# Kernel optimization log

Hardware: AMD Instinct MI355X
Metric: run time of the kernel (lower is better)

Reference implementation:

```python
import jax, jax.numpy as jnp
import numpy as np

B, S, MV = 32, 64, 30
V, E, H, L = 20000, 256, 512, 128
PAD_IDX = 0
THETA = 0.5


def setup_inputs() -> dict:
    key = jax.random.key(0)
    ks = jax.random.split(key, 12)
    sc = 0.02
    return {
        "z": jax.random.normal(ks[0], (B, L), jnp.float32),
        "input_sequence": jax.random.randint(ks[1], (B, S, MV), 0, V),
        "length": jax.random.randint(ks[2], (B,), 1, S + 1),
        "embedding_weight": jax.random.normal(ks[3], (V, E), jnp.float32) * sc,
        "W_l2h": jax.random.normal(ks[4], (H, L), jnp.float32) * sc,
        "b_l2h": jax.random.normal(ks[5], (H,), jnp.float32) * sc,
        "W_ih": jax.random.normal(ks[6], (3 * H, E), jnp.float32) * sc,
        "W_hh": jax.random.normal(ks[7], (3 * H, H), jnp.float32) * sc,
        "b_ih": jax.random.normal(ks[8], (3 * H,), jnp.float32) * sc,
        "b_hh": jax.random.normal(ks[9], (3 * H,), jnp.float32) * sc,
        "W_out": jax.random.normal(ks[10], (V, H), jnp.float32) * sc,
        "b_out": jax.random.normal(ks[11], (V,), jnp.float32) * sc,
    }


def _gru(emb, h0, W_ih, W_hh, b_ih, b_hh):
    # emb: (B,S,E); PyTorch GRU cell, single layer.
    def step(h, x_t):
        gi = x_t @ W_ih.T + b_ih          # (B,3H)
        gh = h @ W_hh.T + b_hh            # (B,3H)
        i_r, i_z, i_n = jnp.split(gi, 3, axis=-1)
        h_r, h_z, h_n = jnp.split(gh, 3, axis=-1)
        r = jax.nn.sigmoid(i_r + h_r)
        zt = jax.nn.sigmoid(i_z + h_z)
        n = jnp.tanh(i_n + r * h_n)
        h_new = (1.0 - zt) * n + zt * h
        return h_new, h_new
    _, outs = jax.lax.scan(step, h0, jnp.swapaxes(emb, 0, 1))  # (S,B,H)
    return jnp.swapaxes(outs, 0, 1)  # (B,S,H)


def reference(z, input_sequence, length, embedding_weight, W_l2h, b_l2h,
              W_ih, W_hh, b_ih, b_hh, W_out, b_out):
    # Multi-hot scatter: zeros.scatter_(2, idx, 1)
    mh = jnp.zeros((B, S, V), jnp.float32).at[
        jnp.arange(B)[:, None, None], jnp.arange(S)[None, :, None], input_sequence
    ].set(1.0)
    mh = mh.at[:, :, PAD_IDX].set(0.0)
    # Dense one-hot matmul embedding-sum (faithful to torch.mm on (B*S,V))
    emb = jnp.tanh(jnp.einsum('bsv,ve->bse', mh, embedding_weight))
    h0 = z @ W_l2h.T + b_l2h                      # (B,H)
    outputs = _gru(emb, h0, W_ih, W_hh, b_ih, b_hh)  # (B,S,H)
    # pack/pad semantics: outputs beyond each length are zero
    valid = jnp.arange(S)[None, :] < length[:, None]
    outputs = outputs * valid[..., None]
    m_output = jnp.sum(jnp.abs(outputs), axis=2) > 0  # (B,S) bool
    logits = jnp.einsum('bsh,vh->bsv', outputs, W_out) + b_out  # (B,S,V)
    p_output = jax.nn.sigmoid(logits)
    # _sample: top-k over logits[..., 3:], shift by 3, threshold via sigmoid
    top_p, top_i = jax.lax.top_k(logits[..., 3:], MV)
    top_i = top_i + 3
    s_output = jnp.where(jax.nn.sigmoid(top_p) <= THETA, PAD_IDX, top_i)  # (B,S,MV)
    return (p_output, s_output, m_output)
```

## Files before the change

### kernel.cpp

```cpp
#include <hip/hip_runtime.h>
#include <hip/hip_bf16.h>
#include <math.h>

#define B_ 32
#define S_ 64
#define MV_ 30
#define V_ 20000
#define E_ 256
#define H_ 512
#define L_ 128
#define H3_ 1536
#define BS_ 2048
#define NB4 256
#define NEG7 -3.0e38f
#define SENT 0xFFF8000000000000ULL

typedef __attribute__((ext_vector_type(8))) short short8v;
typedef __attribute__((ext_vector_type(4))) float f32x4;
typedef unsigned long long ull_;

__global__ __launch_bounds__(256) void k12(const int* __restrict__ seq,
                                           const float* __restrict__ Ew,
                                           const float* __restrict__ z,
                                           const float* __restrict__ Wl,
                                           const float* __restrict__ bl,
                                           double* __restrict__ emb,
                                           double* __restrict__ hstep) {
    __shared__ int sidx[MV_];
    int bid = blockIdx.x;
    int t = threadIdx.x;
    if (bid < BS_) {
        int row = bid;
        if (t < MV_) sidx[t] = seq[row * MV_ + t];
        __syncthreads();
        double acc = 0.0;
        for (int i = 0; i < MV_; ++i) {
            int id = sidx[i];
            if (id == 0) continue;
            bool dup = false;
            for (int q = 0; q < i; ++q) dup = dup || (sidx[q] == id);
            if (!dup) acc += (double)Ew[(size_t)id * E_ + t];
        }
        emb[(size_t)row * E_ + t] = tanh(acc);
    } else if (bid < BS_ + 64) {
        int o = (bid - BS_) * 256 + t;
        int b = o >> 9;
        int j = o & 511;
        const float4* zr = (const float4*)(z + (size_t)b * L_);
        const float4* wr = (const float4*)(Wl + (size_t)j * L_);
        double acc = (double)bl[j];
#pragma unroll
        for (int k = 0; k < L_ / 4; ++k) {
            float4 a = zr[k];
            float4 w = wr[k];
            acc += (double)a.x * (double)w.x + (double)a.y * (double)w.y
                 + (double)a.z * (double)w.z + (double)a.w * (double)w.w;
        }
        hstep[(size_t)(b >> 2) * 2048 + j * 4 + (b & 3)] = acc;
    } else {
        ull_* hs = (ull_*)hstep;
        size_t i = (size_t)(bid - (BS_ + 64)) * 1024 + (size_t)t * 4;
        hs[16384 + i + 0] = SENT;
        hs[16384 + i + 1] = SENT;
        hs[16384 + i + 2] = SENT;
        hs[16384 + i + 3] = SENT;
    }
}

__global__ __launch_bounds__(256) void k3_gi(const double* __restrict__ A,
                                             const float* __restrict__ Bm,
                                             const float* __restrict__ bih,
                                             double* __restrict__ gi) {
    __shared__ double As[16][66];
    __shared__ double Bs[16][66];
    int t = threadIdx.x;
    int n0 = blockIdx.x * 64;
    int m0 = blockIdx.y * 64;
    int tx = t & 15, ty = t >> 4;
    int ml = t >> 2;
    int kl = (t & 3) * 4;
    double acc[4][4];
#pragma unroll
    for (int i = 0; i < 4; ++i)
#pragma unroll
        for (int j = 0; j < 4; ++j) acc[i][j] = 0.0;

    for (int kt = 0; kt < 256; kt += 16) {
        double4 av = *(const double4*)(A + (size_t)(m0 + ml) * 256 + kt + kl);
        float4 bv = *(const float4*)(Bm + (size_t)(n0 + ml) * 256 + kt + kl);
        As[kl + 0][ml] = av.x; As[kl + 1][ml] = av.y; As[kl + 2][ml] = av.z; As[kl + 3][ml] = av.w;
        Bs[kl + 0][ml] = (double)bv.x; Bs[kl + 1][ml] = (double)bv.y;
        Bs[kl + 2][ml] = (double)bv.z; Bs[kl + 3][ml] = (double)bv.w;
        __syncthreads();
#pragma unroll
        for (int kk = 0; kk < 16; ++kk) {
            double2 a01 = *(const double2*)&As[kk][ty * 4];
            double2 a23 = *(const double2*)&As[kk][ty * 4 + 2];
            double2 b01 = *(const double2*)&Bs[kk][tx * 4];
            double2 b23 = *(const double2*)&Bs[kk][tx * 4 + 2];
            double am[4] = {a01.x, a01.y, a23.x, a23.y};
            double bn[4] = {b01.x, b01.y, b23.x, b23.y};
#pragma unroll
            for (int i = 0; i < 4; ++i)
#pragma unroll
                for (int j = 0; j < 4; ++j) acc[i][j] += am[i] * bn[j];
        }
        __syncthreads();
    }
#pragma unroll
    for (int i = 0; i < 4; ++i) {
        int m = m0 + ty * 4 + i;
        int bb = m >> 6, ss = m & 63;
#pragma unroll
        for (int j = 0; j < 4; ++j) {
            int n = n0 + tx * 4 + j;
            int g = n >> 9, u = n & 511;
            gi[(((size_t)(ss * 512 + u)) * 3 + g) * 32 + bb] = acc[i][j] + (double)bih[n];
        }
    }
}

__global__ __launch_bounds__(256, 1) void k4_gru(const double* __restrict__ gi,
                                                 const float* __restrict__ whh,
                                                 const float* __restrict__ bhh,
                                                 const int* __restrict__ length,
                                                 double* __restrict__ hstep,
                                                 float* __restrict__ outs) {
    __shared__ double hl[2112];
    __shared__ double part[2][4][16][13];

    int t = threadIdx.x;
    int wv = t >> 6;
    int lane = t & 63;
    int bid = blockIdx.x;
    int g = bid & 7;
    int beta = bid >> 3;

    int ul = lane >> 2, ks = lane & 3;

    const float* wbase = whh + ((size_t)(beta * 16 + ul)) * 512 + wv * 128 + ks * 32;
    float4 w0r[8], w1r[8], w2r[8];
#pragma unroll
    for (int c = 0; c < 8; ++c) {
        w0r[c] = *(const float4*)(wbase + c * 4);
        w1r[c] = *(const float4*)(wbase + 512 * 512 + c * 4);
        w2r[c] = *(const float4*)(wbase + 1024 * 512 + c * 4);
    }

    const double* hg0 = hstep + (size_t)g * 2048;
    {
#pragma unroll
        for (int j = 0; j < 8; ++j) {
            int e = t + j * 256;
            hl[e + ((e >> 7) << 2)] = hg0[e];
        }
    }
    __syncthreads();

    int u2 = lane >> 2, b2 = lane & 3;
    int u_g = beta * 16 + u2;
    int b_g = g * 4 + b2;
    double gr = 0.0, gz = 0.0, gn = 0.0, bhr_ = 0.0, bhz_ = 0.0, bhn_ = 0.0;
    double hv = 0.0;
    int len = 0;
    if (wv == 0) {
        bhr_ = (double)bhh[u_g];
        bhz_ = (double)bhh[u_g + 512];
        bhn_ = (double)bhh[u_g + 1024];
        len = length[b_g];
        hv = hg0[u_g * 4 + b2];
        size_t gb = ((size_t)u_g * 3) * 32 + b_g;
        gr = gi[gb]; gz = gi[gb + 32]; gn = gi[gb + 64];
    }

    const double* hr = &hl[(wv * 128 + ks * 32) * 4 + ((wv * 4 + ks) << 2)];

    for (int s = 0; s < S_; ++s) {
        int par = s & 1;
        double a0[4] = {0, 0, 0, 0}, a1[4] = {0, 0, 0, 0}, a2[4] = {0, 0, 0, 0};
#pragma unroll
        for (int c = 0; c < 8; ++c) {
            const double* hp = hr + c * 16;
            double2 hA0 = *(const double2*)(hp + 0),  hB0 = *(const double2*)(hp + 2);
            double2 hA1 = *(const double2*)(hp + 4),  hB1 = *(const double2*)(hp + 6);
            double2 hA2 = *(const double2*)(hp + 8),  hB2 = *(const double2*)(hp + 10);
            double2 hA3 = *(const double2*)(hp + 12), hB3 = *(const double2*)(hp + 14);
            float4 w0 = w0r[c], w1 = w1r[c], w2 = w2r[c];
            { double d0 = (double)w0.x, d1 = (double)w1.x, d2 = (double)w2.x;
              a0[0] += hA0.x * d0; a0[1] += hA0.y * d0; a0[2] += hB0.x * d0; a0[3] += hB0.y * d0;
              a1[0] += hA0.x * d1; a1[1] += hA0.y * d1; a1[2] += hB0.x * d1; a1[3] += hB0.y * d1;
              a2[0] += hA0.x * d2; a2[1] += hA0.y * d2; a2[2] += hB0.x * d2; a2[3] += hB0.y * d2; }
            { double d0 = (double)w0.y, d1 = (double)w1.y, d2 = (double)w2.y;
              a0[0] += hA1.x * d0; a0[1] += hA1.y * d0; a0[2] += hB1.x * d0; a0[3] += hB1.y * d0;
              a1[0] += hA1.x * d1; a1[1] += hA1.y * d1; a1[2] += hB1.x * d1; a1[3] += hB1.y * d1;
              a2[0] += hA1.x * d2; a2[1] += hA1.y * d2; a2[2] += hB1.x * d2; a2[3] += hB1.y * d2; }
            { double d0 = (double)w0.z, d1 = (double)w1.z, d2 = (double)w2.z;
              a0[0] += hA2.x * d0; a0[1] += hA2.y * d0; a0[2] += hB2.x * d0; a0[3] += hB2.y * d0;
              a1[0] += hA2.x * d1; a1[1] += hA2.y * d1; a1[2] += hB2.x * d1; a1[3] += hB2.y * d1;
              a2[0] += hA2.x * d2; a2[1] += hA2.y * d2; a2[2] += hB2.x * d2; a2[3] += hB2.y * d2; }
            { double d0 = (double)w0.w, d1 = (double)w1.w, d2 = (double)w2.w;
              a0[0] += hA3.x * d0; a0[1] += hA3.y * d0; a0[2] += hB3.x * d0; a0[3] += hB3.y * d0;
              a1[0] += hA3.x * d1; a1[1] += hA3.y * d1; a1[2] += hB3.x * d1; a1[3] += hB3.y * d1;
              a2[0] += hA3.x * d2; a2[1] += hA3.y * d2; a2[2] += hB3.x * d2; a2[3] += hB3.y * d2; }
        }
#pragma unroll
        for (int b = 0; b < 4; ++b) {
            a0[b] += __shfl_xor(a0[b], 1); a0[b] += __shfl_xor(a0[b], 2);
            a1[b] += __shfl_xor(a1[b], 1); a1[b] += __shfl_xor(a1[b], 2);
            a2[b] += __shfl_xor(a2[b], 1); a2[b] += __shfl_xor(a2[b], 2);
        }
        if (ks == 0) {
#pragma unroll
            for (int b = 0; b < 4; ++b) {
                part[par][wv][ul][0 * 4 + b] = a0[b];
                part[par][wv][ul][1 * 4 + b] = a1[b];
                part[par][wv][ul][2 * 4 + b] = a2[b];
            }
        }
        __syncthreads();

        if (wv == 0) {
            double s0 = part[par][0][u2][0 * 4 + b2] + part[par][1][u2][0 * 4 + b2]
                      + part[par][2][u2][0 * 4 + b2] + part[par][3][u2][0 * 4 + b2];
            double s1 = part[par][0][u2][1 * 4 + b2] + part[par][1][u2][1 * 4 + b2]
                      + part[par][2][u2][1 * 4 + b2] + part[par][3][u2][1 * 4 + b2];
            double s2 = part[par][0][u2][2 * 4 + b2] + part[par][1][u2][2 * 4 + b2]
                      + part[par][2][u2][2 * 4 + b2] + part[par][3][u2][2 * 4 + b2];
            double r  = 1.0 / (1.0 + exp(-(gr + s0 + bhr_)));
            double zt = 1.0 / (1.0 + exp(-(gz + s1 + bhz_)));
            double n  = tanh(gn + r * (s2 + bhn_));
            double hn_ = (1.0 - zt) * n + zt * hv;
            hv = hn_;
            if (s < S_ - 1) {
                ull_* hdst = (ull_*)(hstep + (size_t)(s + 1) * 16384 + (size_t)g * 2048);
                __hip_atomic_store(&hdst[beta * 64 + lane],
                                   __builtin_bit_cast(ull_, hn_),
                                   __ATOMIC_RELAXED, __HIP_MEMORY_SCOPE_AGENT);
                size_t gb = ((size_t)((s + 1) * 512 + u_g) * 3) * 32 + b_g;
                gr = gi[gb]; gz = gi[gb + 32]; gn = gi[gb + 64];
            }
            outs[(size_t)(b_g * 64 + s) * H_ + u_g] = (s < len) ? (float)hn_ : 0.0f;
        }
        if (s == S_ - 1) break;

        {
            const ull_* src = (const ull_*)(hstep + (size_t)(s + 1) * 16384
                                            + (size_t)g * 2048) + wv * 512;
            ull_ tmp[8];
            while (true) {
                bool ok = true;
#pragma unroll
                for (int j = 0; j < 8; ++j) {
                    tmp[j] = __hip_atomic_load(&src[j * 64 + lane],
                                               __ATOMIC_RELAXED, __HIP_MEMORY_SCOPE_AGENT);
                    ok = ok && (tmp[j] != SENT);
                }
                if (__all(ok)) break;
                __builtin_amdgcn_s_sleep(1);
            }
            asm volatile("" ::: "memory");
            ull_* hlu = (ull_*)hl;
#pragma unroll
            for (int j = 0; j < 8; ++j) {
                int e = wv * 512 + j * 64 + lane;
                hlu[e + ((e >> 7) << 2)] = tmp[j];
            }
        }
    }
}

__device__ __forceinline__ unsigned short f2b_(float x) {
    unsigned u = __builtin_bit_cast(unsigned, x);
    return (unsigned short)((u + 0x7FFFu + ((u >> 16) & 1u)) >> 16);
}
__device__ __forceinline__ short8v pack8_(float4 a, float4 b) {
    short8v r;
    r[0] = (short)f2b_(a.x); r[1] = (short)f2b_(a.y);
    r[2] = (short)f2b_(a.z); r[3] = (short)f2b_(a.w);
    r[4] = (short)f2b_(b.x); r[5] = (short)f2b_(b.y);
    r[6] = (short)f2b_(b.z); r[7] = (short)f2b_(b.w);
    return r;
}
__global__ __launch_bounds__(256) void k_prep2(const float* __restrict__ Wsrc,
                                               const float* __restrict__ Asrc,
                                               short* __restrict__ W16,
                                               short* __restrict__ A16) {
    int bid = blockIdx.x, t = threadIdx.x;
    if (bid < 5000) {
        int i = bid * 256 + t;
        float4 a = *(const float4*)&Wsrc[(size_t)i * 8];
        float4 b = *(const float4*)&Wsrc[(size_t)i * 8 + 4];
        *(short8v*)&W16[(size_t)i * 8] = pack8_(a, b);
    } else {
        int i = (bid - 5000) * 256 + t;
        float4 a = *(const float4*)&Asrc[(size_t)i * 8];
        float4 b = *(const float4*)&Asrc[(size_t)i * 8 + 4];
        *(short8v*)&A16[(size_t)i * 8] = pack8_(a, b);
    }
}

#define LDK5 72
__global__ __launch_bounds__(256, 2) void k5_mfma(const short* __restrict__ A16,
                                                  const short* __restrict__ W16,
                                                  const float* __restrict__ bo,
                                                  float* __restrict__ pOut) {
    __shared__ short As[128 * LDK5];
    __shared__ short Bs[128 * LDK5];
    int t = threadIdx.x;
    int bid = blockIdx.x;
    int swz = (bid & 7) * 314 + (bid >> 3);
    int m0 = (swz & 15) * 128;
    int n0 = (swz >> 4) * 128;
    int lane = t & 63, wv = t >> 6;
    int wr = wv >> 1, wc = wv & 1;
    int ml = t >> 1;
    int kl = (t & 1) * 32;

    const short* Arow = A16 + (size_t)(m0 + ml) * H_ + kl;
    int vrow = n0 + ml;
    bool vok = vrow < V_;
    const short* Wrow = W16 + (size_t)(vok ? vrow : 0) * H_ + kl;
    short8v zz = (short8v){0, 0, 0, 0, 0, 0, 0, 0};

    f32x4 acc[4][4];
#pragma unroll
    for (int i = 0; i < 4; ++i)
#pragma unroll
        for (int j = 0; j < 4; ++j) acc[i][j] = (f32x4){0.f, 0.f, 0.f, 0.f};

    int ko = lane >> 4;
    int rr = lane & 15;

    for (int kt = 0; kt < H_; kt += 64) {
        short8v a0 = *(const short8v*)(Arow + kt);
        short8v a1 = *(const short8v*)(Arow + kt + 8);
        short8v a2 = *(const short8v*)(Arow + kt + 16);
        short8v a3 = *(const short8v*)(Arow + kt + 24);
        short8v b0 = vok ? *(const short8v*)(Wrow + kt) : zz;
        short8v b1 = vok ? *(const short8v*)(Wrow + kt + 8) : zz;
        short8v b2 = vok ? *(const short8v*)(Wrow + kt + 16) : zz;
        short8v b3 = vok ? *(const short8v*)(Wrow + kt + 24) : zz;
        *(short8v*)&As[ml * LDK5 + kl]      = a0;
        *(short8v*)&As[ml * LDK5 + kl + 8]  = a1;
        *(short8v*)&As[ml * LDK5 + kl + 16] = a2;
        *(short8v*)&As[ml * LDK5 + kl + 24] = a3;
        *(short8v*)&Bs[ml * LDK5 + kl]      = b0;
        *(short8v*)&Bs[ml * LDK5 + kl + 8]  = b1;
        *(short8v*)&Bs[ml * LDK5 + kl + 16] = b2;
        *(short8v*)&Bs[ml * LDK5 + kl + 24] = b3;
        __syncthreads();

#pragma unroll
        for (int kh = 0; kh < 2; ++kh) {
            short8v af[4], bf[4];
#pragma unroll
            for (int i = 0; i < 4; ++i)
                af[i] = *(const short8v*)&As[(wr * 64 + i * 16 + rr) * LDK5 + kh * 32 + ko * 8];
#pragma unroll
            for (int j = 0; j < 4; ++j)
                bf[j] = *(const short8v*)&Bs[(wc * 64 + j * 16 + rr) * LDK5 + kh * 32 + ko * 8];
#pragma unroll
            for (int i = 0; i < 4; ++i)
#pragma unroll
                for (int j = 0; j < 4; ++j)
                    acc[i][j] = __builtin_amdgcn_mfma_f32_16x16x32_bf16(af[i], bf[j], acc[i][j], 0, 0, 0);
        }
        __syncthreads();
    }

    int cr4 = (lane >> 4) * 4;
    float bov[4];
#pragma unroll
    for (int j = 0; j < 4; ++j) {
        int v = n0 + wc * 64 + j * 16 + rr;
        bov[j] = (v < V_) ? bo[v] : 0.f;
    }
#pragma unroll
    for (int i = 0; i < 4; ++i) {
#pragma unroll
        for (int j = 0; j < 4; ++j) {
            int v = n0 + wc * 64 + j * 16 + rr;
            if (v < V_) {
#pragma unroll
                for (int r = 0; r < 4; ++r) {
                    int m = m0 + wr * 64 + i * 16 + cr4 + r;
                    float x = acc[i][j][r] + bov[j];
                    pOut[(size_t)m * V_ + v] = 1.0f / (1.0f + expf(-x));
                }
            }
        }
    }
}

__global__ __launch_bounds__(512) void k7a_cand(const float* __restrict__ pOut,
                                                float* __restrict__ candV,
                                                int* __restrict__ candI) {
    int row = blockIdx.x;
    int t = threadIdx.x;
    int wv = t >> 6;
    int lane = t & 63;
    const float* rowp = pOut + (size_t)row * V_ + wv * 2500;

    float rv[40];
#pragma unroll
    for (int q4 = 0; q4 < 10; ++q4) {
        int base = q4 * 256 + lane * 4;
        float4 v4 = *(const float4*)(rowp + base);
        float vv[4] = {v4.x, v4.y, v4.z, v4.w};
#pragma unroll
        for (int c = 0; c < 4; ++c) {
            int li = base + c;
            int col = wv * 2500 + li;
            bool ok = (li < 2500) && (col >= 3);
            rv[q4 * 4 + c] = ok ? vv[c] : NEG7;
        }
    }
    float m1 = rv[0]; int s1 = 0;
#pragma unroll
    for (int q = 1; q < 40; ++q)
        if (rv[q] > m1) { m1 = rv[q]; s1 = q; }
    float m2 = NEG7; int s2 = 0;
#pragma unroll
    for (int q = 0; q < 40; ++q)
        if (q != s1 && rv[q] > m2) { m2 = rv[q]; s2 = q; }
    bool dirty = false;
    ull_ used = 0;
    int myidx = wv * 2500 + (s1 >> 2) * 256 + lane * 4 + (s1 & 3);

    float keepv = NEG7; int keepi = 0;
#pragma unroll 1
    for (int r = 0; r < 32; ++r) {
        float bv = m1; int bi = myidx;
#pragma unroll
        for (int m = 1; m < 64; m <<= 1) {
            float ov = __shfl_xor(bv, m);
            int   oi = __shfl_xor(bi, m);
            if (ov > bv || (ov == bv && oi < bi)) { bv = ov; bi = oi; }
        }
        if (lane == r) { keepv = bv; keepi = bi; }
        if (myidx == bi) {
            used |= (1ull << s1);
            if (!dirty) {
                m1 = m2; s1 = s2; dirty = true;
            } else {
                m1 = NEG7; s1 = 0;
#pragma unroll
                for (int q = 0; q < 40; ++q) {
                    float v = ((used >> q) & 1ull) ? NEG7 : rv[q];
                    if (v > m1) { m1 = v; s1 = q; }
                }
                m2 = NEG7; s2 = 0;
#pragma unroll
                for (int q = 0; q < 40; ++q) {
                    float v = (((used >> q) & 1ull) || q == s1) ? NEG7 : rv[q];
                    if (v > m2) { m2 = v; s2 = q; }
                }
                dirty = false;
            }
            myidx = wv * 2500 + (s1 >> 2) * 256 + lane * 4 + (s1 & 3);
        }
    }
    if (lane < 32) {
        size_t o = ((size_t)row * 8 + wv) * 32 + lane;
        candV[o] = keepv;
        candI[o] = keepi;
    }
}

__global__ __launch_bounds__(256) void k7b_final(const float* __restrict__ candV,
                                                 const int* __restrict__ candI,
                                                 const float* __restrict__ outs,
                                                 const float* __restrict__ W,
                                                 const float* __restrict__ bo,
                                                 float* __restrict__ mOut,
                                                 float* __restrict__ sOut) {
    __shared__ float selv[64];
    __shared__ int   seli[64];
    __shared__ float resv[64];
    __shared__ float redm[4];
    __shared__ __align__(16) float orow[H_];

    int row = blockIdx.x;
    int t = threadIdx.x;
    int lane = t & 63, wid = t >> 6;

    if (wid != 0) {
        for (int i = t - 64; i < H_; i += 192)
            orow[i] = outs[(size_t)row * H_ + i];
    } else {
        float cv[4]; int ci[4];
#pragma unroll
        for (int q = 0; q < 4; ++q) {
            size_t o = (size_t)row * 256 + q * 64 + lane;
            cv[q] = candV[o];
            ci[q] = candI[o];
        }
        float lv = cv[0]; int lix = ci[0]; int ls = 0;
#pragma unroll
        for (int q = 1; q < 4; ++q)
            if (cv[q] > lv || (cv[q] == lv && ci[q] < lix)) { lv = cv[q]; lix = ci[q]; ls = q; }

#pragma unroll 1
        for (int r = 0; r < 64; ++r) {
            float bv = lv; int bi = lix;
#pragma unroll
            for (int m = 1; m < 64; m <<= 1) {
                float ov = __shfl_xor(bv, m);
                int   oi = __shfl_xor(bi, m);
                if (ov > bv || (ov == bv && oi < bi)) { bv = ov; bi = oi; }
            }
            if (lane == r) { selv[r] = bv; seli[r] = bi; }
            if (lix == bi) {
#pragma unroll
                for (int q = 0; q < 4; ++q) cv[q] = (ls == q) ? NEG7 : cv[q];
                lv = cv[0]; lix = ci[0]; ls = 0;
#pragma unroll
                for (int q = 1; q < 4; ++q)
                    if (cv[q] > lv || (cv[q] == lv && ci[q] < lix)) { lv = cv[q]; lix = ci[q]; ls = q; }
            }
        }
    }
    __syncthreads();

    {
        float ms = fabsf(orow[t]) + fabsf(orow[t + 256]);
#pragma unroll
        for (int m = 1; m < 64; m <<= 1) ms += __shfl_xor(ms, m);
        if (lane == 0) redm[wid] = ms;
    }

    {
        int c = t >> 2, q = t & 3;
        int gidx = seli[c];
        const float4* w4 = (const float4*)(W + (size_t)gidx * H_);
        const float4* o4 = (const float4*)orow;
        double acc = 0.0;
#pragma unroll 8
        for (int i2 = 0; i2 < 32; ++i2) {
            float4 wv4 = w4[i2 * 4 + q];
            float4 ov4 = o4[i2 * 4 + q];
            acc += (double)wv4.x * (double)ov4.x + (double)wv4.y * (double)ov4.y
                 + (double)wv4.z * (double)ov4.z + (double)wv4.w * (double)ov4.w;
        }
        acc += __shfl_xor(acc, 1);
        acc += __shfl_xor(acc, 2);
        if (q == 0) resv[c] = (float)(acc + (double)bo[gidx]);
    }
    __syncthreads();

    if (t == 0)
        mOut[row] = (redm[0] + redm[1] + redm[2] + redm[3] > 0.f) ? 1.f : 0.f;

    if (t < 64) {
        float v = resv[t];
        int idx = seli[t];
#pragma unroll 1
        for (int r = 0; r < MV_; ++r) {
            float bv = v; int bi = idx;
#pragma unroll
            for (int m = 1; m < 64; m <<= 1) {
                float ov = __shfl_xor(bv, m);
                int   oi = __shfl_xor(bi, m);
                if (ov > bv || (ov == bv && oi < bi)) { bv = ov; bi = oi; }
            }
            if (t == 0)
                sOut[(size_t)row * MV_ + r] = (bv <= 0.0f) ? 0.0f : (float)bi;
            if (idx == bi) v = NEG7;
        }
    }
}

extern "C" void kernel_launch(void* const* d_in, const int* in_sizes, int n_in,
                              void* d_out, int out_size, void* d_ws, size_t ws_size,
                              hipStream_t stream) {
    const float* z      = (const float*)d_in[0];
    const int*   seq    = (const int*)d_in[1];
    const int*   length = (const int*)d_in[2];
    const float* Ew     = (const float*)d_in[3];
    const float* W_l2h  = (const float*)d_in[4];
    const float* b_l2h  = (const float*)d_in[5];
    const float* W_ih   = (const float*)d_in[6];
    const float* W_hh   = (const float*)d_in[7];
    const float* b_ih   = (const float*)d_in[8];
    const float* b_hh   = (const float*)d_in[9];
    const float* W_out  = (const float*)d_in[10];
    const float* b_out  = (const float*)d_in[11];

    float* out = (float*)d_out;

    double* emb_d = (double*)d_ws;
    double* gi_d  = emb_d + 524288;
    double* hstep = gi_d + 3145728;
    float*  outs  = (float*)(hstep + 1048576);
    float*  candV = outs + 1048576;
    int*    candI = (int*)(candV + (size_t)BS_ * 256);
    short*  A16   = (short*)emb_d;
    short*  W16   = (short*)gi_d;

    float* pOut = out;
    float* sOut = out + (size_t)BS_ * V_;
    float* mOut = sOut + (size_t)BS_ * MV_;

    k12<<<BS_ + 64 + 1008, 256, 0, stream>>>(seq, Ew, z, W_l2h, b_l2h, emb_d, hstep);
    k3_gi<<<dim3(24, 32), 256, 0, stream>>>(emb_d, W_ih, b_ih, gi_d);
    k4_gru<<<NB4, 256, 0, stream>>>(gi_d, W_hh, b_hh, length, hstep, outs);
    k_prep2<<<5512, 256, 0, stream>>>(W_out, outs, W16, A16);
    k5_mfma<<<2512, 256, 0, stream>>>(A16, W16, b_out, pOut);
    k7a_cand<<<BS_, 512, 0, stream>>>(pOut, candV, candI);
    k7b_final<<<BS_, 256, 0, stream>>>(candV, candI, outs, W_out, b_out, mOut, sOut);
}
```

Measured before the change: 658.6 us.

## Split hidden-state polling into halves overlapped with partial recurrent matvec

Moves the cross-block polling for the next hidden state to the top of each timestep and splits it in two. Each lane now loads only the h slice its own wave reads. The first half of the slice is waited on before the first four chunks of the matvec, and the second half is prefetched and checked afterwards. This overlaps the global spin-wait and load latency for the second half with computation on the first half. The cost is more complex synchronization, and the removed __syncthreads-free reuse assumes each lane only reads the LDS entries it wrote itself.

```diff
diff --git a/kernel.cpp b/kernel.cpp
--- a/kernel.cpp
+++ b/kernel.cpp
@@ -174,12 +174,43 @@
     }
 
     const double* hr = &hl[(wv * 128 + ks * 32) * 4 + ((wv * 4 + ks) << 2)];
+    int sbase = ks * 128 + ul * 4;
 
     for (int s = 0; s < S_; ++s) {
         int par = s & 1;
+        ull_ ta[4], tb[4];
+        const ull_* src = (const ull_*)(hstep + (size_t)s * 16384 + (size_t)g * 2048)
+                          + wv * 512;
+        if (s > 0) {
+            while (true) {
+                bool ok = true;
+#pragma unroll
+                for (int j = 0; j < 4; ++j) {
+                    ta[j] = __hip_atomic_load(&src[sbase + j], __ATOMIC_RELAXED,
+                                              __HIP_MEMORY_SCOPE_AGENT);
+                    ok = ok && (ta[j] != SENT);
+                }
+                if (__all(ok)) break;
+                __builtin_amdgcn_s_sleep(1);
+            }
+#pragma unroll
+            for (int j = 0; j < 4; ++j)
+                tb[j] = __hip_atomic_load(&src[sbase + 64 + j], __ATOMIC_RELAXED,
+                                          __HIP_MEMORY_SCOPE_AGENT);
+            asm volatile("" ::: "memory");
+            {
+                ull_* hlu = (ull_*)hl;
+#pragma unroll
+                for (int j = 0; j < 4; ++j) {
+                    int e = wv * 512 + sbase + j;
+                    hlu[e + ((e >> 7) << 2)] = ta[j];
+                }
+            }
+        }
+
         double a0[4] = {0, 0, 0, 0}, a1[4] = {0, 0, 0, 0}, a2[4] = {0, 0, 0, 0};
 #pragma unroll
-        for (int c = 0; c < 8; ++c) {
+        for (int c = 0; c < 4; ++c) {
             const double* hp = hr + c * 16;
             double2 hA0 = *(const double2*)(hp + 0),  hB0 = *(const double2*)(hp + 2);
             double2 hA1 = *(const double2*)(hp + 4),  hB1 = *(const double2*)(hp + 6);
@@ -203,6 +234,56 @@
               a1[0] += hA3.x * d1; a1[1] += hA3.y * d1; a1[2] += hB3.x * d1; a1[3] += hB3.y * d1;
               a2[0] += hA3.x * d2; a2[1] += hA3.y * d2; a2[2] += hB3.x * d2; a2[3] += hB3.y * d2; }
         }
+
+        if (s > 0) {
+            while (true) {
+                bool ok = true;
+#pragma unroll
+                for (int j = 0; j < 4; ++j) ok = ok && (tb[j] != SENT);
+                if (__all(ok)) break;
+                __builtin_amdgcn_s_sleep(1);
+#pragma unroll
+                for (int j = 0; j < 4; ++j)
+                    tb[j] = __hip_atomic_load(&src[sbase + 64 + j], __ATOMIC_RELAXED,
+                                              __HIP_MEMORY_SCOPE_AGENT);
+            }
+            asm volatile("" ::: "memory");
+            {
+                ull_* hlu = (ull_*)hl;
+#pragma unroll
+                for (int j = 0; j < 4; ++j) {
+                    int e = wv * 512 + sbase + 64 + j;
+                    hlu[e + ((e >> 7) << 2)] = tb[j];
+                }
+            }
+        }
+
+#pragma unroll
+        for (int c = 4; c < 8; ++c) {
+            const double* hp = hr + c * 16;
+            double2 hA0 = *(const double2*)(hp + 0),  hB0 = *(const double2*)(hp + 2);
+            double2 hA1 = *(const double2*)(hp + 4),  hB1 = *(const double2*)(hp + 6);
+            double2 hA2 = *(const double2*)(hp + 8),  hB2 = *(const double2*)(hp + 10);
+            double2 hA3 = *(const double2*)(hp + 12), hB3 = *(const double2*)(hp + 14);
+            float4 w0 = w0r[c], w1 = w1r[c], w2 = w2r[c];
+            { double d0 = (double)w0.x, d1 = (double)w1.x, d2 = (double)w2.x;
+              a0[0] += hA0.x * d0; a0[1] += hA0.y * d0; a0[2] += hB0.x * d0; a0[3] += hB0.y * d0;
+              a1[0] += hA0.x * d1; a1[1] += hA0.y * d1; a1[2] += hB0.x * d1; a1[3] += hB0.y * d1;
+              a2[0] += hA0.x * d2; a2[1] += hA0.y * d2; a2[2] += hB0.x * d2; a2[3] += hB0.y * d2; }
+            { double d0 = (double)w0.y, d1 = (double)w1.y, d2 = (double)w2.y;
+              a0[0] += hA1.x * d0; a0[1] += hA1.y * d0; a0[2] += hB1.x * d0; a0[3] += hB1.y * d0;
+              a1[0] += hA1.x * d1; a1[1] += hA1.y * d1; a1[2] += hB1.x * d1; a1[3] += hB1.y * d1;
+              a2[0] += hA1.x * d2; a2[1] += hA1.y * d2; a2[2] += hB1.x * d2; a2[3] += hB1.y * d2; }
+            { double d0 = (double)w0.z, d1 = (double)w1.z, d2 = (double)w2.z;
+              a0[0] += hA2.x * d0; a0[1] += hA2.y * d0; a0[2] += hB2.x * d0; a0[3] += hB2.y * d0;
+              a1[0] += hA2.x * d1; a1[1] += hA2.y * d1; a1[2] += hB2.x * d1; a1[3] += hB2.y * d1;
+              a2[0] += hA2.x * d2; a2[1] += hA2.y * d2; a2[2] += hB2.x * d2; a2[3] += hB2.y * d2; }
+            { double d0 = (double)w0.w, d1 = (double)w1.w, d2 = (double)w2.w;
+              a0[0] += hA3.x * d0; a0[1] += hA3.y * d0; a0[2] += hB3.x * d0; a0[3] += hB3.y * d0;
+              a1[0] += hA3.x * d1; a1[1] += hA3.y * d1; a1[2] += hB3.x * d1; a1[3] += hB3.y * d1;
+              a2[0] += hA3.x * d2; a2[1] += hA3.y * d2; a2[2] += hB3.x * d2; a2[3] += hB3.y * d2; }
+        }
+
 #pragma unroll
         for (int b = 0; b < 4; ++b) {
             a0[b] += __shfl_xor(a0[b], 1); a0[b] += __shfl_xor(a0[b], 2);
@@ -241,31 +322,6 @@
             }
             outs[(size_t)(b_g * 64 + s) * H_ + u_g] = (s < len) ? (float)hn_ : 0.0f;
         }
-        if (s == S_ - 1) break;
-
-        {
-            const ull_* src = (const ull_*)(hstep + (size_t)(s + 1) * 16384
-                                            + (size_t)g * 2048) + wv * 512;
-            ull_ tmp[8];
-            while (true) {
-                bool ok = true;
-#pragma unroll
-                for (int j = 0; j < 8; ++j) {
-                    tmp[j] = __hip_atomic_load(&src[j * 64 + lane],
-                                               __ATOMIC_RELAXED, __HIP_MEMORY_SCOPE_AGENT);
-                    ok = ok && (tmp[j] != SENT);
-                }
-                if (__all(ok)) break;
-                __builtin_amdgcn_s_sleep(1);
-            }
-            asm volatile("" ::: "memory");
-            ull_* hlu = (ull_*)hl;
-#pragma unroll
-            for (int j = 0; j < 8; ++j) {
-                int e = wv * 512 + j * 64 + lane;
-                hlu[e + ((e >> 7) << 2)] = tmp[j];
-            }
-        }
     }
 }
 
```

Measured after the change: 697.5 us. 5.9% more time.
